# Kernel optimization log

Measured on AMD Instinct MI355X. Metric: run time of the kernel, lower is better.

## Reference

```python
import jax, jax.numpy as jnp
import numpy as np

N_NODES = 100000
N_EDGES = 1600000
N_GRAPHS = 256
IN_DIM, HID = 30, 40

def setup_inputs() -> dict:
    key = jax.random.key(0)
    ks = jax.random.split(key, 12)
    x = jax.random.normal(ks[0], (N_NODES, IN_DIM), dtype=jnp.float32)
    edge_index = jax.random.randint(ks[1], (2, N_EDGES), 0, N_NODES, dtype=jnp.int64)
    batch = jnp.sort(jax.random.randint(ks[2], (N_NODES,), 0, N_GRAPHS, dtype=jnp.int64))
    def glorot(k, shape):
        lim = float(np.sqrt(6.0 / (shape[0] + shape[1])))
        return jax.random.uniform(k, shape, dtype=jnp.float32, minval=-lim, maxval=lim)
    return {
        'x': x, 'edge_index': edge_index, 'batch': batch,
        'W1': glorot(ks[3], (IN_DIM, HID)), 'b1': jnp.zeros((HID,), jnp.float32),
        'W2': glorot(ks[4], (HID, HID)),    'b2': jnp.zeros((HID,), jnp.float32),
        'W3': glorot(ks[5], (HID, HID)),    'b3': jnp.zeros((HID,), jnp.float32),
        'lin_w': glorot(ks[6], (HID, 1)),   'lin_b': jnp.zeros((1,), jnp.float32),
    }

def _gcn_layer(x, src, dst, norm, W, b, n_nodes):
    # x: [N, Fin] -> [N, Fout]; fused gather-matmul-scatter form of GCNConv
    h = x @ W                                   # dense transform first (Fout small)
    msg = h[src] * norm[:, None]                # [E+N, Fout] gather + edge scale
    out = jax.ops.segment_sum(msg, dst, num_segments=n_nodes)
    return out + b

def reference(x, edge_index, batch, W1, b1, W2, b2, W3, b3, lin_w, lin_b):
    n = x.shape[0]
    loops = jnp.arange(n, dtype=edge_index.dtype)
    src = jnp.concatenate([edge_index[0], loops])  # add self loops (GCNConv default)
    dst = jnp.concatenate([edge_index[1], loops])
    deg = jax.ops.segment_sum(jnp.ones_like(dst, dtype=x.dtype), dst, num_segments=n)
    dinv = jax.lax.rsqrt(jnp.maximum(deg, 1.0))    # deg >= 1 thanks to self loops
    norm = dinv[src] * dinv[dst]

    h = jax.nn.relu(_gcn_layer(x, src, dst, norm, W1, b1, n))  # dropout inactive (eval)
    h = jax.nn.relu(_gcn_layer(h, src, dst, norm, W2, b2, n))
    h = jax.nn.relu(_gcn_layer(h, src, dst, norm, W3, b3, n))

    # global_mean_pool over graphs
    g_sum = jax.ops.segment_sum(h, batch, num_segments=N_GRAPHS)
    cnt = jax.ops.segment_sum(jnp.ones((n,), h.dtype), batch, num_segments=N_GRAPHS)
    g = g_sum / jnp.maximum(cnt, 1.0)[:, None]
    return g @ lin_w + lin_b                      # [N_GRAPHS, 1]
```

## Files before the change

kernel.cpp:

```cpp
#include <hip/hip_runtime.h>

#define HID 40
#define RBKT 196
#define BSH 9
#define CAP 12288
#define EPB 4096


typedef __attribute__((ext_vector_type(4))) unsigned uv4;
typedef __attribute__((ext_vector_type(8))) __bf16 bf16x8;
typedef __attribute__((ext_vector_type(8))) unsigned short usv8;
typedef __attribute__((ext_vector_type(4))) float f32x4;

__device__ inline unsigned pack2_bf16(float a, float b) {
    unsigned ua = __float_as_uint(a);
    unsigned ub = __float_as_uint(b);
    ua = (ua + 0x7fffu + ((ua >> 16) & 1u)) >> 16;
    ub = (ub + 0x7fffu + ((ub >> 16) & 1u)) & 0xffff0000u;
    return ua | ub;
}

__device__ inline void acc8_bf16(float* acc, uint4 v) {
    acc[0] += __uint_as_float(v.x << 16);
    acc[1] += __uint_as_float(v.x & 0xffff0000u);
    acc[2] += __uint_as_float(v.y << 16);
    acc[3] += __uint_as_float(v.y & 0xffff0000u);
    acc[4] += __uint_as_float(v.z << 16);
    acc[5] += __uint_as_float(v.z & 0xffff0000u);
    acc[6] += __uint_as_float(v.w << 16);
    acc[7] += __uint_as_float(v.w & 0xffff0000u);
}

__global__ void clear_kernel(int* __restrict__ bucket_cnt, float* __restrict__ g_sum, int G) {
    int t = blockIdx.x * blockDim.x + threadIdx.x;
    if (t < RBKT) bucket_cnt[t] = 0;
    if (t < G) g_sum[t] = 0.f;
}


__global__ __launch_bounds__(256) void binA_kernel(
        const int* __restrict__ esrc, const int* __restrict__ edst, int E,
        int* __restrict__ bucket_cnt, int* __restrict__ bucket_data) {
    __shared__ int cnt_l[RBKT];
    __shared__ int base_l[RBKT];
    int t = threadIdx.x;
    for (int b = t; b < RBKT; b += 256) cnt_l[b] = 0;
    __syncthreads();
    int e0 = blockIdx.x * EPB;
    int e1 = min(e0 + EPB, E);
    for (int e = e0 + t; e < e1; e += 256) {
        atomicAdd(&cnt_l[edst[e] >> BSH], 1);
    }
    __syncthreads();
    for (int b = t; b < RBKT; b += 256) {
        int c = cnt_l[b];
        base_l[b] = (c > 0) ? atomicAdd(&bucket_cnt[b], c) : 0;
        cnt_l[b] = 0;
    }
    __syncthreads();
    for (int e = e0 + t; e < e1; e += 256) {
        int d = edst[e];
        int s = esrc[e];
        int b = d >> BSH;
        int off = base_l[b] + atomicAdd(&cnt_l[b], 1);
        if (off < CAP) bucket_data[(size_t)b * CAP + off] = (s << BSH) | (d & 511);
    }
}

__global__ void scan_buckets_kernel(const int* __restrict__ cnt, int* __restrict__ base) {
    __shared__ int s[256];
    int t = threadIdx.x;
    int c = (t < RBKT) ? min(cnt[t], CAP) : 0;
    s[t] = c;
    __syncthreads();
    for (int off = 1; off < 256; off <<= 1) {
        int y = (t >= off) ? s[t - off] : 0;
        __syncthreads();
        s[t] += y;
        __syncthreads();
    }
    if (t < RBKT) base[t] = s[t] - c;
    if (t == RBKT - 1) base[RBKT] = s[t];
}

__global__ __launch_bounds__(256) void buildB_kernel(
        const int* __restrict__ bucket_cnt, const int* __restrict__ bucket_base,
        const int* __restrict__ bucket_data,
        int* __restrict__ rowptr, int* __restrict__ mid, int* __restrict__ csr,
        float* __restrict__ dinv, int n, int half) {
    __shared__ int deg_l[512];
    __shared__ int deg_lo[512];
    __shared__ int off_lo[512];
    __shared__ int off_hi[512];
    __shared__ int ps[256];
    int r = blockIdx.x;
    int t = threadIdx.x;
    int cnt = min(bucket_cnt[r], CAP);
    int base = bucket_base[r];
    int node0 = r << BSH;
    int nr = min(512, n - node0);
    for (int i = t; i < 512; i += 256) { deg_l[i] = 0; deg_lo[i] = 0; }
    __syncthreads();
    const int* data = bucket_data + (size_t)r * CAP;
    for (int e = t; e < cnt; e += 256) {
        int v = data[e];
        atomicAdd(&deg_l[v & 511], 1);
        if ((v >> BSH) < half) atomicAdd(&deg_lo[v & 511], 1);
    }
    __syncthreads();
    int a0 = deg_l[2 * t], a1 = deg_l[2 * t + 1];
    ps[t] = a0 + a1;
    __syncthreads();
    for (int off = 1; off < 256; off <<= 1) {
        int y = (t >= off) ? ps[t - off] : 0;
        __syncthreads();
        ps[t] += y;
        __syncthreads();
    }
    int excl = ps[t] - (a0 + a1);
    off_lo[2 * t] = excl;
    off_lo[2 * t + 1] = excl + a0;
    off_hi[2 * t] = excl + deg_lo[2 * t];
    off_hi[2 * t + 1] = excl + a0 + deg_lo[2 * t + 1];
    __syncthreads();
    for (int i = t; i < nr; i += 256) {
        int rp = base + off_lo[i];
        rowptr[node0 + i] = rp;
        mid[node0 + i] = rp + deg_lo[i];
        dinv[node0 + i] = rsqrtf((float)(deg_l[i] + 1));
    }
    if (r == RBKT - 1 && t == 0) rowptr[n] = base + cnt;
    __syncthreads();
    for (int e = t; e < cnt; e += 256) {
        int v = data[e];
        int s = v >> BSH;
        int d = v & 511;
        int p = (s < half) ? atomicAdd(&off_lo[d], 1) : atomicAdd(&off_hi[d], 1);
        csr[base + p] = s;
    }
}


__global__ __launch_bounds__(256) void scale_bf16_kernel(
        const float* __restrict__ x, const float* __restrict__ dinv,
        unsigned* __restrict__ xs, int n) {
    int t = blockIdx.x * blockDim.x + threadIdx.x;
    int i = t >> 4, p = t & 15;
    if (i >= n) return;
    float a = 0.f, b = 0.f;
    if (p < 15) {
        float d = dinv[i];
        a = x[i * 30 + 2 * p] * d;
        b = x[i * 30 + 2 * p + 1] * d;
    }
    xs[(size_t)i * 16 + p] = pack2_bf16(a, b);
}

template <int TPN>
__global__ __launch_bounds__(256) void gather_bf16_kernel(
        const unsigned* __restrict__ xs, const int* __restrict__ rowptr,
        const int* __restrict__ mid, const int* __restrict__ csr,
        const float* __restrict__ dinv, unsigned* __restrict__ gout, int n) {
    int t = blockIdx.x * blockDim.x + threadIdx.x;
    int i = t / TPN;
    int q = t - i * TPN;
    if (i >= n) return;
    const uint4* tab = reinterpret_cast<const uint4*>(xs);
    float acc[8];
    {
        uint4 v = tab[(size_t)i * TPN + q];
        acc[0] = __uint_as_float(v.x << 16);
        acc[1] = __uint_as_float(v.x & 0xffff0000u);
        acc[2] = __uint_as_float(v.y << 16);
        acc[3] = __uint_as_float(v.y & 0xffff0000u);
        acc[4] = __uint_as_float(v.z << 16);
        acc[5] = __uint_as_float(v.z & 0xffff0000u);
        acc[6] = __uint_as_float(v.w << 16);
        acc[7] = __uint_as_float(v.w & 0xffff0000u);
    }
    int e0 = rowptr[i], m = mid[i], e1 = rowptr[i + 1];
    int e = e0;
    for (; e + 4 <= m; e += 4) {
        int s0 = csr[e], s1 = csr[e + 1], s2 = csr[e + 2], s3 = csr[e + 3];
        uint4 v0 = tab[(size_t)s0 * TPN + q];
        uint4 v1 = tab[(size_t)s1 * TPN + q];
        uint4 v2 = tab[(size_t)s2 * TPN + q];
        uint4 v3 = tab[(size_t)s3 * TPN + q];
        acc8_bf16(acc, v0);
        acc8_bf16(acc, v1);
        acc8_bf16(acc, v2);
        acc8_bf16(acc, v3);
    }
    for (; e < m; e++) acc8_bf16(acc, tab[(size_t)csr[e] * TPN + q]);
    for (; e + 4 <= e1; e += 4) {
        int s0 = csr[e], s1 = csr[e + 1], s2 = csr[e + 2], s3 = csr[e + 3];
        uint4 v0 = tab[(size_t)s0 * TPN + q];
        uint4 v1 = tab[(size_t)s1 * TPN + q];
        uint4 v2 = tab[(size_t)s2 * TPN + q];
        uint4 v3 = tab[(size_t)s3 * TPN + q];
        acc8_bf16(acc, v0);
        acc8_bf16(acc, v1);
        acc8_bf16(acc, v2);
        acc8_bf16(acc, v3);
    }
    for (; e < e1; e++) acc8_bf16(acc, tab[(size_t)csr[e] * TPN + q]);
    float d = dinv[i];
    uint4 o;
    o.x = pack2_bf16(acc[0] * d, acc[1] * d);
    o.y = pack2_bf16(acc[2] * d, acc[3] * d);
    o.z = pack2_bf16(acc[4] * d, acc[5] * d);
    o.w = pack2_bf16(acc[6] * d, acc[7] * d);
    reinterpret_cast<uint4*>(gout)[(size_t)i * TPN + q] = o;
}

template <int INF>
__global__ void wprep_kernel(const float* __restrict__ W, unsigned* __restrict__ wtab) {
    constexpr int KST = (INF > 32) ? 2 : 1;
    int l = threadIdx.x;
    int lr = l & 15, lg = l >> 4;
    for (int kst = 0; kst < KST; kst++) {
        for (int ct = 0; ct < 3; ct++) {
            unsigned short v[8];
            #pragma unroll
            for (int i = 0; i < 8; i++) {
                int kb = kst * 32 + lg * 8 + i;
                int col = ct * 16 + lr;
                float f = (kb < INF && col < 40) ? W[kb * 40 + col] : 0.f;
                v[i] = (unsigned short)(pack2_bf16(f, 0.f) & 0xffffu);
            }
            uint4 u;
            u.x = (unsigned)v[0] | ((unsigned)v[1] << 16);
            u.y = (unsigned)v[2] | ((unsigned)v[3] << 16);
            u.z = (unsigned)v[4] | ((unsigned)v[5] << 16);
            u.w = (unsigned)v[6] | ((unsigned)v[7] << 16);
            reinterpret_cast<uint4*>(wtab)[(kst * 3 + ct) * 64 + l] = u;
        }
    }
}

template <int INF, int RQ, bool POOL>
__global__ __launch_bounds__(256) void transform_mfma_kernel(
        const unsigned* __restrict__ tin, const unsigned* __restrict__ wtab,
        const float* __restrict__ bias, const float* __restrict__ dinv,
        const float* __restrict__ lin_w, const int* __restrict__ batch,
        unsigned* __restrict__ out, float* __restrict__ g_sum, int n) {
    constexpr int KST = (INF > 32) ? 2 : 1;
    __shared__ float sarr[POOL ? 64 : 1];
    __shared__ unsigned ost[POOL ? 1 : 64 * 21];
    const int tid = threadIdx.x;
    const int wv = tid >> 6;
    const int l = tid & 63;
    const int lr = l & 15;
    const int lg = l >> 4;
    const uv4* wt = reinterpret_cast<const uv4*>(wtab);
    usv8 wf[KST][3];
    #pragma unroll
    for (int kst = 0; kst < KST; kst++) {
        #pragma unroll
        for (int ct = 0; ct < 3; ct++) {
            wf[kst][ct] = __builtin_bit_cast(usv8, wt[(kst * 3 + ct) * 64 + l]);
        }
    }
    const int node0 = blockIdx.x * 64 + wv * 16;
    const uv4* tab = reinterpret_cast<const uv4*>(tin);
    const int arow = node0 + lr;
    uv4 zq = {0u, 0u, 0u, 0u};
    uv4 a0q = (arow < n) ? tab[(size_t)arow * RQ + lg] : zq;
    bf16x8 a0 = __builtin_bit_cast(bf16x8, a0q);
    bf16x8 a1;
    if constexpr (KST == 2) {
        uv4 a1q = (arow < n && lg == 0) ? tab[(size_t)arow * RQ + 4] : zq;
        a1 = __builtin_bit_cast(bf16x8, a1q);
    }
    f32x4 acc[3];
    #pragma unroll
    for (int ct = 0; ct < 3; ct++) {
        f32x4 z = {0.f, 0.f, 0.f, 0.f};
        acc[ct] = __builtin_amdgcn_mfma_f32_16x16x32_bf16(
            a0, __builtin_bit_cast(bf16x8, wf[0][ct]), z, 0, 0, 0);
        if constexpr (KST == 2) {
            acc[ct] = __builtin_amdgcn_mfma_f32_16x16x32_bf16(
                a1, __builtin_bit_cast(bf16x8, wf[1][ct]), acc[ct], 0, 0, 0);
        }
    }
    int noder[4]; float dr[4]; bool vr[4];
    #pragma unroll
    for (int r = 0; r < 4; r++) {
        noder[r] = node0 + lg * 4 + r;
        vr[r] = (noder[r] < n);
        dr[r] = vr[r] ? dinv[noder[r]] : 0.f;
    }
    if (!POOL) {
        #pragma unroll
        for (int ct = 0; ct < 3; ct++) {
            int col = ct * 16 + lr;
            float bc = (col < 40) ? bias[col] : 0.f;
            #pragma unroll
            for (int r = 0; r < 4; r++) {
                float v = fmaxf(acc[ct][r] + bc, 0.f) * dr[r];
                float pv = __shfl_xor(v, 1, 64);
                if (((lr & 1) == 0) && col < 40) {
                    int nl = wv * 16 + lg * 4 + r;
                    ost[nl * 21 + ct * 8 + (lr >> 1)] = pack2_bf16(v, pv);
                }
            }
        }
        __syncthreads();
        int blk0 = blockIdx.x * 64;
        int nr = min(64, n - blk0);
        int tot = nr * 5;
        uint4* outq = reinterpret_cast<uint4*>(out) + (size_t)blk0 * 5;
        for (int idx = tid; idx < tot; idx += 256) {
            int nl = idx / 5, c4 = idx - nl * 5;
            uint4 v;
            v.x = ost[nl * 21 + c4 * 4 + 0];
            v.y = ost[nl * 21 + c4 * 4 + 1];
            v.z = ost[nl * 21 + c4 * 4 + 2];
            v.w = ost[nl * 21 + c4 * 4 + 3];
            outq[idx] = v;
        }
    } else {
        float s[4] = {0.f, 0.f, 0.f, 0.f};
        #pragma unroll
        for (int ct = 0; ct < 3; ct++) {
            int col = ct * 16 + lr;
            float bc = (col < 40) ? bias[col] : 0.f;
            float lwv = (col < 40) ? lin_w[col] : 0.f;
            #pragma unroll
            for (int r = 0; r < 4; r++)
                s[r] += fmaxf(acc[ct][r] + bc, 0.f) * lwv;
        }
        #pragma unroll
        for (int r = 0; r < 4; r++) if (!vr[r]) s[r] = 0.f;
        #pragma unroll
        for (int mask = 1; mask <= 8; mask <<= 1) {
            #pragma unroll
            for (int r = 0; r < 4; r++) s[r] += __shfl_xor(s[r], mask, 64);
        }
        if (lr == 0) {
            #pragma unroll
            for (int r = 0; r < 4; r++) sarr[wv * 16 + lg * 4 + r] = s[r];
        }
        __syncthreads();
        if (tid < 64) {
            float ss = sarr[tid];
            int node2 = blockIdx.x * 64 + tid;
            bool v2 = (node2 < n);
            int gg = batch[v2 ? node2 : (n - 1)];
            if (!v2) ss = 0.f;
            int g0 = __shfl(gg, 0, 64);
            if (__all(gg == g0)) {
                #pragma unroll
                for (int off2 = 32; off2 > 0; off2 >>= 1) ss += __shfl_xor(ss, off2, 64);
                if (tid == 0) atomicAdd(&g_sum[g0], ss);
            } else {
                if (v2) atomicAdd(&g_sum[gg], ss);
            }
        }
    }
}

__global__ void finalize_kernel(const float* __restrict__ g_sum,
                                const int* __restrict__ batch,
                                const float* __restrict__ lin_b,
                                float* __restrict__ out, int n, int G) {
    int b = blockIdx.x * blockDim.x + threadIdx.x;
    if (b >= G) return;
    int lo = 0, hi = n;
    while (lo < hi) { int m = (lo + hi) >> 1; if (batch[m] < b) lo = m + 1; else hi = m; }
    int lo2 = lo, hi2 = n;
    while (lo2 < hi2) { int m = (lo2 + hi2) >> 1; if (batch[m] < b + 1) lo2 = m + 1; else hi2 = m; }
    int cnt = lo2 - lo;
    out[b] = g_sum[b] / (float)(cnt > 0 ? cnt : 1) + lin_b[0];
}


static inline size_t align_up(size_t v, size_t a) { return (v + a - 1) / a * a; }

extern "C" void kernel_launch(void* const* d_in, const int* in_sizes, int n_in,
                              void* d_out, int out_size, void* d_ws, size_t ws_size,
                              hipStream_t stream) {
    const float* x      = (const float*)d_in[0];
    const int*   esrc   = (const int*)d_in[1];
    const int*   batch  = (const int*)d_in[2];
    const float* W1     = (const float*)d_in[3];
    const float* b1     = (const float*)d_in[4];
    const float* W2     = (const float*)d_in[5];
    const float* b2     = (const float*)d_in[6];
    const float* W3     = (const float*)d_in[7];
    const float* b3     = (const float*)d_in[8];
    const float* lin_w  = (const float*)d_in[9];
    const float* lin_b  = (const float*)d_in[10];
    float* out = (float*)d_out;

    const int n = in_sizes[0] / 30;
    const int E = in_sizes[1] / 2;
    const int G = out_size;
    const int* edst = esrc + E;

    char* w = (char*)d_ws;
    size_t off = 0;
    auto take = [&](size_t bytes) { size_t o = off; off = align_up(off + bytes, 256); return (void*)(w + o); };
    int*      bucket_cnt  = (int*)take((size_t)RBKT * 4);
    int*      bucket_base = (int*)take((size_t)(RBKT + 1) * 4);
    int*      rowptr      = (int*)take((size_t)(n + 1) * 4);
    int*      mid         = (int*)take((size_t)n * 4);
    float*    dinv        = (float*)take((size_t)n * 4);
    int*      csr         = (int*)take((size_t)E * 4);
    float*    g_sum       = (float*)take((size_t)G * 4);
    unsigned* wtab1       = (unsigned*)take((size_t)3 * 64 * 16);
    unsigned* wtab2       = (unsigned*)take((size_t)6 * 64 * 16);
    unsigned* wtab3       = (unsigned*)take((size_t)6 * 64 * 16);
    size_t bd = (size_t)RBKT * CAP * 4;
    size_t x1 = (size_t)n * 16 * 4;
    void* shared_region = take(bd > x1 ? bd : x1);
    int*      bucket_data = (int*)shared_region;
    unsigned* xs1         = (unsigned*)shared_region;
    unsigned* agg         = (unsigned*)take((size_t)n * 20 * 4);
    unsigned* tbA         = (unsigned*)take((size_t)n * 20 * 4);
    unsigned* tbB         = (unsigned*)take((size_t)n * 20 * 4);
    (void)ws_size;

    clear_kernel<<<1, 256, 0, stream>>>(bucket_cnt, g_sum, G);

    binA_kernel<<<(E + EPB - 1) / EPB, 256, 0, stream>>>(esrc, edst, E, bucket_cnt, bucket_data);
    scan_buckets_kernel<<<1, 256, 0, stream>>>(bucket_cnt, bucket_base);
    buildB_kernel<<<RBKT, 256, 0, stream>>>(bucket_cnt, bucket_base, bucket_data,
                                            rowptr, mid, csr, dinv, n, n / 2);

    wprep_kernel<30><<<1, 64, 0, stream>>>(W1, wtab1);
    wprep_kernel<40><<<1, 64, 0, stream>>>(W2, wtab2);
    wprep_kernel<40><<<1, 64, 0, stream>>>(W3, wtab3);

    int nblkT = (n + 63) / 64;

    scale_bf16_kernel<<<((size_t)n * 16 + 255) / 256, 256, 0, stream>>>(x, dinv, xs1, n);
    gather_bf16_kernel<4><<<((size_t)n * 4 + 255) / 256, 256, 0, stream>>>(
        xs1, rowptr, mid, csr, dinv, agg, n);
    transform_mfma_kernel<30, 4, false><<<nblkT, 256, 0, stream>>>(
        agg, wtab1, b1, dinv, nullptr, nullptr, tbA, nullptr, n);
    gather_bf16_kernel<5><<<((size_t)n * 5 + 255) / 256, 256, 0, stream>>>(
        tbA, rowptr, mid, csr, dinv, agg, n);
    transform_mfma_kernel<40, 5, false><<<nblkT, 256, 0, stream>>>(
        agg, wtab2, b2, dinv, nullptr, nullptr, tbB, nullptr, n);
    gather_bf16_kernel<5><<<((size_t)n * 5 + 255) / 256, 256, 0, stream>>>(
        tbB, rowptr, mid, csr, dinv, agg, n);
    transform_mfma_kernel<40, 5, true><<<nblkT, 256, 0, stream>>>(
        agg, wtab3, b3, dinv, lin_w, batch, nullptr, g_sum, n);

    finalize_kernel<<<1, 256, 0, stream>>>(g_sum, batch, lin_b, out, n, G);
}
```

Baseline: 204.7 us.

## Fuse gather and MFMA transform per layer, merge weight prep into clear kernel

Each GCN layer now runs its neighbour gather/aggregation into a shared-memory tile and then does the MFMA transform in the same block. This removes the intermediate agg buffer round-trip through global memory and three kernel launches. The three weight-prep launches are also folded into the clear kernel, so each runs in a separate wavefront. In exchange, the MFMA phase uses only four of the five waves in RQ=5 blocks, and the block size changes to 320 threads. Gather and transform can no longer overlap across separate kernels.

```diff
diff --git a/kernel.cpp b/kernel.cpp
--- a/kernel.cpp
+++ b/kernel.cpp
@@ -31,10 +31,42 @@
     acc[7] += __uint_as_float(v.w & 0xffff0000u);
 }
 
-__global__ void clear_kernel(int* __restrict__ bucket_cnt, float* __restrict__ g_sum, int G) {
-    int t = blockIdx.x * blockDim.x + threadIdx.x;
+__device__ inline void wprep_dev(const float* __restrict__ W,
+                                 unsigned* __restrict__ wtab, int INF, int l) {
+    int lr = l & 15, lg = l >> 4;
+    int kstn = (INF > 32) ? 2 : 1;
+    for (int kst = 0; kst < kstn; kst++) {
+        for (int ct = 0; ct < 3; ct++) {
+            unsigned short v[8];
+            #pragma unroll
+            for (int i = 0; i < 8; i++) {
+                int kb = kst * 32 + lg * 8 + i;
+                int col = ct * 16 + lr;
+                float f = (kb < INF && col < 40) ? W[kb * 40 + col] : 0.f;
+                v[i] = (unsigned short)(pack2_bf16(f, 0.f) & 0xffffu);
+            }
+            uint4 u;
+            u.x = (unsigned)v[0] | ((unsigned)v[1] << 16);
+            u.y = (unsigned)v[2] | ((unsigned)v[3] << 16);
+            u.z = (unsigned)v[4] | ((unsigned)v[5] << 16);
+            u.w = (unsigned)v[6] | ((unsigned)v[7] << 16);
+            reinterpret_cast<uint4*>(wtab)[(kst * 3 + ct) * 64 + l] = u;
+        }
+    }
+}
+
+__global__ void prep_kernel(int* __restrict__ bucket_cnt, float* __restrict__ g_sum, int G,
+                            const float* __restrict__ W1, const float* __restrict__ W2,
+                            const float* __restrict__ W3,
+                            unsigned* __restrict__ wtab1, unsigned* __restrict__ wtab2,
+                            unsigned* __restrict__ wtab3) {
+    int t = threadIdx.x;
     if (t < RBKT) bucket_cnt[t] = 0;
     if (t < G) g_sum[t] = 0.f;
+    int w = t >> 6, l = t & 63;
+    if (w == 1) wprep_dev(W1, wtab1, 30, l);
+    else if (w == 2) wprep_dev(W2, wtab2, 40, l);
+    else if (w == 3) wprep_dev(W3, wtab3, 40, l);
 }
 
 
@@ -156,161 +188,161 @@
     xs[(size_t)i * 16 + p] = pack2_bf16(a, b);
 }
 
-template <int TPN>
-__global__ __launch_bounds__(256) void gather_bf16_kernel(
-        const unsigned* __restrict__ xs, const int* __restrict__ rowptr,
-        const int* __restrict__ mid, const int* __restrict__ csr,
-        const float* __restrict__ dinv, unsigned* __restrict__ gout, int n) {
-    int t = blockIdx.x * blockDim.x + threadIdx.x;
-    int i = t / TPN;
-    int q = t - i * TPN;
-    if (i >= n) return;
-    const uint4* tab = reinterpret_cast<const uint4*>(xs);
-    float acc[8];
-    {
-        uint4 v = tab[(size_t)i * TPN + q];
-        acc[0] = __uint_as_float(v.x << 16);
-        acc[1] = __uint_as_float(v.x & 0xffff0000u);
-        acc[2] = __uint_as_float(v.y << 16);
-        acc[3] = __uint_as_float(v.y & 0xffff0000u);
-        acc[4] = __uint_as_float(v.z << 16);
-        acc[5] = __uint_as_float(v.z & 0xffff0000u);
-        acc[6] = __uint_as_float(v.w << 16);
-        acc[7] = __uint_as_float(v.w & 0xffff0000u);
-    }
-    int e0 = rowptr[i], m = mid[i], e1 = rowptr[i + 1];
-    int e = e0;
-    for (; e + 4 <= m; e += 4) {
-        int s0 = csr[e], s1 = csr[e + 1], s2 = csr[e + 2], s3 = csr[e + 3];
-        uint4 v0 = tab[(size_t)s0 * TPN + q];
-        uint4 v1 = tab[(size_t)s1 * TPN + q];
-        uint4 v2 = tab[(size_t)s2 * TPN + q];
-        uint4 v3 = tab[(size_t)s3 * TPN + q];
-        acc8_bf16(acc, v0);
-        acc8_bf16(acc, v1);
-        acc8_bf16(acc, v2);
-        acc8_bf16(acc, v3);
-    }
-    for (; e < m; e++) acc8_bf16(acc, tab[(size_t)csr[e] * TPN + q]);
-    for (; e + 4 <= e1; e += 4) {
-        int s0 = csr[e], s1 = csr[e + 1], s2 = csr[e + 2], s3 = csr[e + 3];
-        uint4 v0 = tab[(size_t)s0 * TPN + q];
-        uint4 v1 = tab[(size_t)s1 * TPN + q];
-        uint4 v2 = tab[(size_t)s2 * TPN + q];
-        uint4 v3 = tab[(size_t)s3 * TPN + q];
-        acc8_bf16(acc, v0);
-        acc8_bf16(acc, v1);
-        acc8_bf16(acc, v2);
-        acc8_bf16(acc, v3);
-    }
-    for (; e < e1; e++) acc8_bf16(acc, tab[(size_t)csr[e] * TPN + q]);
-    float d = dinv[i];
-    uint4 o;
-    o.x = pack2_bf16(acc[0] * d, acc[1] * d);
-    o.y = pack2_bf16(acc[2] * d, acc[3] * d);
-    o.z = pack2_bf16(acc[4] * d, acc[5] * d);
-    o.w = pack2_bf16(acc[6] * d, acc[7] * d);
-    reinterpret_cast<uint4*>(gout)[(size_t)i * TPN + q] = o;
-}
-
-template <int INF>
-__global__ void wprep_kernel(const float* __restrict__ W, unsigned* __restrict__ wtab) {
-    constexpr int KST = (INF > 32) ? 2 : 1;
-    int l = threadIdx.x;
-    int lr = l & 15, lg = l >> 4;
-    for (int kst = 0; kst < KST; kst++) {
-        for (int ct = 0; ct < 3; ct++) {
-            unsigned short v[8];
-            #pragma unroll
-            for (int i = 0; i < 8; i++) {
-                int kb = kst * 32 + lg * 8 + i;
-                int col = ct * 16 + lr;
-                float f = (kb < INF && col < 40) ? W[kb * 40 + col] : 0.f;
-                v[i] = (unsigned short)(pack2_bf16(f, 0.f) & 0xffffu);
-            }
-            uint4 u;
-            u.x = (unsigned)v[0] | ((unsigned)v[1] << 16);
-            u.y = (unsigned)v[2] | ((unsigned)v[3] << 16);
-            u.z = (unsigned)v[4] | ((unsigned)v[5] << 16);
-            u.w = (unsigned)v[6] | ((unsigned)v[7] << 16);
-            reinterpret_cast<uint4*>(wtab)[(kst * 3 + ct) * 64 + l] = u;
-        }
-    }
-}
-
 template <int INF, int RQ, bool POOL>
-__global__ __launch_bounds__(256) void transform_mfma_kernel(
-        const unsigned* __restrict__ tin, const unsigned* __restrict__ wtab,
-        const float* __restrict__ bias, const float* __restrict__ dinv,
-        const float* __restrict__ lin_w, const int* __restrict__ batch,
+__global__ __launch_bounds__(64 * RQ) void fused_layer_kernel(
+        const unsigned* __restrict__ xs, const unsigned* __restrict__ wtab,
+        const int* __restrict__ rowptr, const int* __restrict__ mid,
+        const int* __restrict__ csr, const float* __restrict__ dinv,
+        const float* __restrict__ bias, const float* __restrict__ lin_w,
+        const int* __restrict__ batch,
         unsigned* __restrict__ out, float* __restrict__ g_sum, int n) {
     constexpr int KST = (INF > 32) ? 2 : 1;
+    constexpr int NT  = 64 * RQ;
+    constexpr int TS  = (RQ == 4) ? 5 : 7;
+    __shared__ uint4 tile[64 * TS];
     __shared__ float sarr[POOL ? 64 : 1];
     __shared__ unsigned ost[POOL ? 1 : 64 * 21];
     const int tid = threadIdx.x;
-    const int wv = tid >> 6;
-    const int l = tid & 63;
-    const int lr = l & 15;
-    const int lg = l >> 4;
-    const uv4* wt = reinterpret_cast<const uv4*>(wtab);
-    usv8 wf[KST][3];
-    #pragma unroll
-    for (int kst = 0; kst < KST; kst++) {
+
+    {
+        const int node_l = tid / RQ, q = tid - node_l * RQ;
+        const int gi = blockIdx.x * 64 + node_l;
+        if (gi < n) {
+            const uint4* tab = reinterpret_cast<const uint4*>(xs);
+            float acc[8];
+            {
+                uint4 v = tab[(size_t)gi * RQ + q];
+                acc[0] = __uint_as_float(v.x << 16);
+                acc[1] = __uint_as_float(v.x & 0xffff0000u);
+                acc[2] = __uint_as_float(v.y << 16);
+                acc[3] = __uint_as_float(v.y & 0xffff0000u);
+                acc[4] = __uint_as_float(v.z << 16);
+                acc[5] = __uint_as_float(v.z & 0xffff0000u);
+                acc[6] = __uint_as_float(v.w << 16);
+                acc[7] = __uint_as_float(v.w & 0xffff0000u);
+            }
+            int e0 = rowptr[gi], m = mid[gi], e1 = rowptr[gi + 1];
+            int e = e0;
+            for (; e + 4 <= m; e += 4) {
+                int s0 = csr[e], s1 = csr[e + 1], s2 = csr[e + 2], s3 = csr[e + 3];
+                uint4 v0 = tab[(size_t)s0 * RQ + q];
+                uint4 v1 = tab[(size_t)s1 * RQ + q];
+                uint4 v2 = tab[(size_t)s2 * RQ + q];
+                uint4 v3 = tab[(size_t)s3 * RQ + q];
+                acc8_bf16(acc, v0);
+                acc8_bf16(acc, v1);
+                acc8_bf16(acc, v2);
+                acc8_bf16(acc, v3);
+            }
+            for (; e < m; e++) acc8_bf16(acc, tab[(size_t)csr[e] * RQ + q]);
+            for (; e + 4 <= e1; e += 4) {
+                int s0 = csr[e], s1 = csr[e + 1], s2 = csr[e + 2], s3 = csr[e + 3];
+                uint4 v0 = tab[(size_t)s0 * RQ + q];
+                uint4 v1 = tab[(size_t)s1 * RQ + q];
+                uint4 v2 = tab[(size_t)s2 * RQ + q];
+                uint4 v3 = tab[(size_t)s3 * RQ + q];
+                acc8_bf16(acc, v0);
+                acc8_bf16(acc, v1);
+                acc8_bf16(acc, v2);
+                acc8_bf16(acc, v3);
+            }
+            for (; e < e1; e++) acc8_bf16(acc, tab[(size_t)csr[e] * RQ + q]);
+            float d = dinv[gi];
+            uint4 o;
+            o.x = pack2_bf16(acc[0] * d, acc[1] * d);
+            o.y = pack2_bf16(acc[2] * d, acc[3] * d);
+            o.z = pack2_bf16(acc[4] * d, acc[5] * d);
+            o.w = pack2_bf16(acc[6] * d, acc[7] * d);
+            tile[node_l * TS + q] = o;
+        }
+    }
+    __syncthreads();
+
+    const int wv = tid >> 6, l = tid & 63, lr = l & 15, lg = l >> 4;
+    if (wv < 4) {
+        const uv4* wt = reinterpret_cast<const uv4*>(wtab);
+        usv8 wf[KST][3];
+        #pragma unroll
+        for (int kst = 0; kst < KST; kst++) {
+            #pragma unroll
+            for (int ct = 0; ct < 3; ct++) {
+                wf[kst][ct] = __builtin_bit_cast(usv8, wt[(kst * 3 + ct) * 64 + l]);
+            }
+        }
+        const int node0 = blockIdx.x * 64 + wv * 16;
+        const int arow_l = wv * 16 + lr;
+        bf16x8 a0 = __builtin_bit_cast(bf16x8, tile[arow_l * TS + lg]);
+        bf16x8 a1;
+        if constexpr (KST == 2) {
+            uint4 z4 = {0u, 0u, 0u, 0u};
+            uint4 a1q = (lg == 0) ? tile[arow_l * TS + 4] : z4;
+            a1 = __builtin_bit_cast(bf16x8, a1q);
+        }
+        f32x4 acc[3];
         #pragma unroll
         for (int ct = 0; ct < 3; ct++) {
-            wf[kst][ct] = __builtin_bit_cast(usv8, wt[(kst * 3 + ct) * 64 + l]);
-        }
-    }
-    const int node0 = blockIdx.x * 64 + wv * 16;
-    const uv4* tab = reinterpret_cast<const uv4*>(tin);
-    const int arow = node0 + lr;
-    uv4 zq = {0u, 0u, 0u, 0u};
-    uv4 a0q = (arow < n) ? tab[(size_t)arow * RQ + lg] : zq;
-    bf16x8 a0 = __builtin_bit_cast(bf16x8, a0q);
-    bf16x8 a1;
-    if constexpr (KST == 2) {
-        uv4 a1q = (arow < n && lg == 0) ? tab[(size_t)arow * RQ + 4] : zq;
-        a1 = __builtin_bit_cast(bf16x8, a1q);
-    }
-    f32x4 acc[3];
-    #pragma unroll
-    for (int ct = 0; ct < 3; ct++) {
-        f32x4 z = {0.f, 0.f, 0.f, 0.f};
-        acc[ct] = __builtin_amdgcn_mfma_f32_16x16x32_bf16(
-            a0, __builtin_bit_cast(bf16x8, wf[0][ct]), z, 0, 0, 0);
-        if constexpr (KST == 2) {
+            f32x4 z = {0.f, 0.f, 0.f, 0.f};
             acc[ct] = __builtin_amdgcn_mfma_f32_16x16x32_bf16(
-                a1, __builtin_bit_cast(bf16x8, wf[1][ct]), acc[ct], 0, 0, 0);
-        }
-    }
-    int noder[4]; float dr[4]; bool vr[4];
-    #pragma unroll
-    for (int r = 0; r < 4; r++) {
-        noder[r] = node0 + lg * 4 + r;
-        vr[r] = (noder[r] < n);
-        dr[r] = vr[r] ? dinv[noder[r]] : 0.f;
-    }
+                a0, __builtin_bit_cast(bf16x8, wf[0][ct]), z, 0, 0, 0);
+            if constexpr (KST == 2) {
+                acc[ct] = __builtin_amdgcn_mfma_f32_16x16x32_bf16(
+                    a1, __builtin_bit_cast(bf16x8, wf[1][ct]), acc[ct], 0, 0, 0);
+            }
+        }
+        int noder[4]; float dr[4]; bool vr[4];
+        #pragma unroll
+        for (int r = 0; r < 4; r++) {
+            noder[r] = node0 + lg * 4 + r;
+            vr[r] = (noder[r] < n);
+            dr[r] = vr[r] ? dinv[noder[r]] : 0.f;
+        }
+        if (!POOL) {
+            #pragma unroll
+            for (int ct = 0; ct < 3; ct++) {
+                int col = ct * 16 + lr;
+                float bc = (col < 40) ? bias[col] : 0.f;
+                #pragma unroll
+                for (int r = 0; r < 4; r++) {
+                    float v = fmaxf(acc[ct][r] + bc, 0.f) * dr[r];
+                    float pv = __shfl_xor(v, 1, 64);
+                    if (((lr & 1) == 0) && col < 40) {
+                        int nl = wv * 16 + lg * 4 + r;
+                        ost[nl * 21 + ct * 8 + (lr >> 1)] = pack2_bf16(v, pv);
+                    }
+                }
+            }
+        } else {
+            float s[4] = {0.f, 0.f, 0.f, 0.f};
+            #pragma unroll
+            for (int ct = 0; ct < 3; ct++) {
+                int col = ct * 16 + lr;
+                float bc = (col < 40) ? bias[col] : 0.f;
+                float lwv = (col < 40) ? lin_w[col] : 0.f;
+                #pragma unroll
+                for (int r = 0; r < 4; r++)
+                    s[r] += fmaxf(acc[ct][r] + bc, 0.f) * lwv;
+            }
+            #pragma unroll
+            for (int r = 0; r < 4; r++) if (!vr[r]) s[r] = 0.f;
+            #pragma unroll
+            for (int mask = 1; mask <= 8; mask <<= 1) {
+                #pragma unroll
+                for (int r = 0; r < 4; r++) s[r] += __shfl_xor(s[r], mask, 64);
+            }
+            if (lr == 0) {
+                #pragma unroll
+                for (int r = 0; r < 4; r++) sarr[wv * 16 + lg * 4 + r] = s[r];
+            }
+        }
+    }
+    __syncthreads();
+
     if (!POOL) {
-        #pragma unroll
-        for (int ct = 0; ct < 3; ct++) {
-            int col = ct * 16 + lr;
-            float bc = (col < 40) ? bias[col] : 0.f;
-            #pragma unroll
-            for (int r = 0; r < 4; r++) {
-                float v = fmaxf(acc[ct][r] + bc, 0.f) * dr[r];
-                float pv = __shfl_xor(v, 1, 64);
-                if (((lr & 1) == 0) && col < 40) {
-                    int nl = wv * 16 + lg * 4 + r;
-                    ost[nl * 21 + ct * 8 + (lr >> 1)] = pack2_bf16(v, pv);
-                }
-            }
-        }
-        __syncthreads();
         int blk0 = blockIdx.x * 64;
         int nr = min(64, n - blk0);
         int tot = nr * 5;
         uint4* outq = reinterpret_cast<uint4*>(out) + (size_t)blk0 * 5;
-        for (int idx = tid; idx < tot; idx += 256) {
+        for (int idx = tid; idx < tot; idx += NT) {
             int nl = idx / 5, c4 = idx - nl * 5;
             uint4 v;
             v.x = ost[nl * 21 + c4 * 4 + 0];
@@ -320,28 +352,6 @@
             outq[idx] = v;
         }
     } else {
-        float s[4] = {0.f, 0.f, 0.f, 0.f};
-        #pragma unroll
-        for (int ct = 0; ct < 3; ct++) {
-            int col = ct * 16 + lr;
-            float bc = (col < 40) ? bias[col] : 0.f;
-            float lwv = (col < 40) ? lin_w[col] : 0.f;
-            #pragma unroll
-            for (int r = 0; r < 4; r++)
-                s[r] += fmaxf(acc[ct][r] + bc, 0.f) * lwv;
-        }
-        #pragma unroll
-        for (int r = 0; r < 4; r++) if (!vr[r]) s[r] = 0.f;
-        #pragma unroll
-        for (int mask = 1; mask <= 8; mask <<= 1) {
-            #pragma unroll
-            for (int r = 0; r < 4; r++) s[r] += __shfl_xor(s[r], mask, 64);
-        }
-        if (lr == 0) {
-            #pragma unroll
-            for (int r = 0; r < 4; r++) sarr[wv * 16 + lg * 4 + r] = s[r];
-        }
-        __syncthreads();
         if (tid < 64) {
             float ss = sarr[tid];
             int node2 = blockIdx.x * 64 + tid;
@@ -416,37 +426,27 @@
     void* shared_region = take(bd > x1 ? bd : x1);
     int*      bucket_data = (int*)shared_region;
     unsigned* xs1         = (unsigned*)shared_region;
-    unsigned* agg         = (unsigned*)take((size_t)n * 20 * 4);
     unsigned* tbA         = (unsigned*)take((size_t)n * 20 * 4);
     unsigned* tbB         = (unsigned*)take((size_t)n * 20 * 4);
     (void)ws_size;
 
-    clear_kernel<<<1, 256, 0, stream>>>(bucket_cnt, g_sum, G);
+    prep_kernel<<<1, 256, 0, stream>>>(bucket_cnt, g_sum, G, W1, W2, W3,
+                                       wtab1, wtab2, wtab3);
 
     binA_kernel<<<(E + EPB - 1) / EPB, 256, 0, stream>>>(esrc, edst, E, bucket_cnt, bucket_data);
     scan_buckets_kernel<<<1, 256, 0, stream>>>(bucket_cnt, bucket_base);
     buildB_kernel<<<RBKT, 256, 0, stream>>>(bucket_cnt, bucket_base, bucket_data,
                                             rowptr, mid, csr, dinv, n, n / 2);
 
-    wprep_kernel<30><<<1, 64, 0, stream>>>(W1, wtab1);
-    wprep_kernel<40><<<1, 64, 0, stream>>>(W2, wtab2);
-    wprep_kernel<40><<<1, 64, 0, stream>>>(W3, wtab3);
-
-    int nblkT = (n + 63) / 64;
+    int nblk = (n + 63) / 64;
 
     scale_bf16_kernel<<<((size_t)n * 16 + 255) / 256, 256, 0, stream>>>(x, dinv, xs1, n);
-    gather_bf16_kernel<4><<<((size_t)n * 4 + 255) / 256, 256, 0, stream>>>(
-        xs1, rowptr, mid, csr, dinv, agg, n);
-    transform_mfma_kernel<30, 4, false><<<nblkT, 256, 0, stream>>>(
-        agg, wtab1, b1, dinv, nullptr, nullptr, tbA, nullptr, n);
-    gather_bf16_kernel<5><<<((size_t)n * 5 + 255) / 256, 256, 0, stream>>>(
-        tbA, rowptr, mid, csr, dinv, agg, n);
-    transform_mfma_kernel<40, 5, false><<<nblkT, 256, 0, stream>>>(
-        agg, wtab2, b2, dinv, nullptr, nullptr, tbB, nullptr, n);
-    gather_bf16_kernel<5><<<((size_t)n * 5 + 255) / 256, 256, 0, stream>>>(
-        tbB, rowptr, mid, csr, dinv, agg, n);
-    transform_mfma_kernel<40, 5, true><<<nblkT, 256, 0, stream>>>(
-        agg, wtab3, b3, dinv, lin_w, batch, nullptr, g_sum, n);
+    fused_layer_kernel<30, 4, false><<<nblk, 256, 0, stream>>>(
+        xs1, wtab1, rowptr, mid, csr, dinv, b1, nullptr, nullptr, tbA, nullptr, n);
+    fused_layer_kernel<40, 5, false><<<nblk, 320, 0, stream>>>(
+        tbA, wtab2, rowptr, mid, csr, dinv, b2, nullptr, nullptr, tbB, nullptr, n);
+    fused_layer_kernel<40, 5, true><<<nblk, 320, 0, stream>>>(
+        tbB, wtab3, rowptr, mid, csr, dinv, b3, lin_w, batch, nullptr, g_sum, n);
 
     finalize_kernel<<<1, 256, 0, stream>>>(g_sum, batch, lin_b, out, n, G);
 }
```

Measured after the change: 196.3 us (median of 2 runs). 4.1% less time.
